# Kernel tuning notes

Hardware: AMD Instinct MI355X
Metric: run time of the kernel (lower is better)

The kernel has to match this reference:

```python
import jax, jax.numpy as jnp
import numpy as np

EMBED_DIM = 1024
NUM_HEADS = 16
HEAD_DIM = EMBED_DIM // NUM_HEADS
FF_DIM = 4096
SPARSITY_FACTOR = 0.1
SPARSITY_THRESHOLD = 0.5
EPS = 1e-5


def layer_norm(x, w, b):
    mu = jnp.mean(x, axis=-1, keepdims=True)
    var = jnp.mean(jnp.square(x - mu), axis=-1, keepdims=True)
    return (x - mu) * jax.lax.rsqrt(var + EPS) * w + b


def setup_inputs() -> dict:
    key = jax.random.key(0)
    ks = jax.random.split(key, 12)
    B, N, C = 8, 1024, EMBED_DIM
    s = 0.02
    return {
        "x": jax.random.normal(ks[0], (B, N, C), jnp.float32),
        "ln1_w": jnp.ones((C,), jnp.float32),
        "ln1_b": jnp.zeros((C,), jnp.float32),
        "qkv_w": jax.random.normal(ks[1], (3 * C, C), jnp.float32) * s,
        "qkv_b": jnp.zeros((3 * C,), jnp.float32),
        "out_w": jax.random.normal(ks[2], (C, C), jnp.float32) * s,
        "out_b": jnp.zeros((C,), jnp.float32),
        "ln2_w": jnp.ones((C,), jnp.float32),
        "ln2_b": jnp.zeros((C,), jnp.float32),
        "w1": jax.random.normal(ks[3], (FF_DIM, C), jnp.float32) * s,
        "b1": jnp.zeros((FF_DIM,), jnp.float32),
        "w2": jax.random.normal(ks[4], (C, FF_DIM), jnp.float32) * s,
        "b2": jnp.zeros((C,), jnp.float32),
        "mask1": jax.random.uniform(ks[5], (B, N, FF_DIM), jnp.float32),
        "mask2": jax.random.uniform(ks[6], (B, N, C), jnp.float32),
        "layer_idx": 0,
    }


def sparse_attention(x, qkv_w, qkv_b, out_w, out_b):
    B, N, C = x.shape
    qkv = (x @ qkv_w.T + qkv_b).reshape(B, N, 3, NUM_HEADS, HEAD_DIM)
    qkv = jnp.transpose(qkv, (2, 0, 3, 1, 4))  # (3,B,H,N,hd)
    q, k, v = qkv[0], qkv[1], qkv[2]
    scale = HEAD_DIM ** (-0.5)
    scores = jnp.einsum("bhnd,bhmd->bhnm", q, k) * scale  # (B,H,N,N)
    k_sparse = int(SPARSITY_FACTOR * N)
    if 0 < k_sparse < N:
        _, idx = jax.lax.top_k(scores, k_sparse)  # (B,H,N,k)
        bi = jnp.arange(B)[:, None, None, None]
        hi = jnp.arange(NUM_HEADS)[None, :, None, None]
        ni = jnp.arange(N)[None, None, :, None]
        mask = jnp.zeros_like(scores).at[bi, hi, ni, idx].set(1.0)
        scores = scores * mask - 1e9 * (1.0 - mask)
    attn = jax.nn.softmax(scores, axis=-1)
    out = jnp.einsum("bhnm,bhmd->bhnd", attn, v)  # (B,H,N,hd)
    out = jnp.transpose(out, (0, 2, 1, 3)).reshape(B, N, C)
    return out @ out_w.T + out_b


def reference(x, ln1_w, ln1_b, qkv_w, qkv_b, out_w, out_b, ln2_w, ln2_b,
              w1, b1, w2, b2, mask1, mask2, layer_idx):
    # Attention block with residual
    x = x + sparse_attention(layer_norm(x, ln1_w, ln1_b), qkv_w, qkv_b, out_w, out_b)
    # Random-masked FFN block with residual
    m1 = (mask1 > SPARSITY_THRESHOLD).astype(x.dtype)
    m2 = (mask2 > SPARSITY_THRESHOLD).astype(x.dtype)
    h = layer_norm(x, ln2_w, ln2_b)
    h = jax.nn.relu((h @ w1.T + b1) * m1)
    h = ((h @ w2.T + b2) * m2)
    x = x + h
    # Symbolic branch: only runs when (layer_idx+1)%4==0 and never modifies x
    # (original ends in `pass`), so it is an identity on the output.
    return x
```

## Files before the change

### kernel.cpp

```cpp
#include <hip/hip_runtime.h>
#include <cstdint>
#include <cstddef>

typedef unsigned short u16;
typedef __bf16 bf16x8 __attribute__((ext_vector_type(8)));
typedef float f32x4 __attribute__((ext_vector_type(4)));

#define GLOBAL_AS __attribute__((address_space(1)))
#define LDS_AS    __attribute__((address_space(3)))

__device__ __forceinline__ float bf2f(u16 v) {
  return __builtin_bit_cast(float, (uint32_t)v << 16);
}
__device__ __forceinline__ u16 f2bf(float f) {
  uint32_t u = __builtin_bit_cast(uint32_t, f);
  u += 0x7FFFu + ((u >> 16) & 1u);
  return (u16)(u >> 16);
}
__device__ __forceinline__ float extload(const void* p, size_t i, int isf) {
  return isf ? ((const float*)p)[i] : bf2f(((const u16*)p)[i]);
}
__device__ __forceinline__ void gl_lds16(const void* g, void* l) {
  __builtin_amdgcn_global_load_lds((const GLOBAL_AS void*)g, (LDS_AS void*)l, 16, 0, 0);
}

__global__ __launch_bounds__(256) void sniff_k(const u16* __restrict__ x, int* __restrict__ flag) {
  const int t = threadIdx.x;
  int cnt = 0;
#pragma unroll
  for (int j = 0; j < 16; ++j) {
    const u16 w = x[t * 16 + j];
    const int e = (w >> 7) & 0xFF;
    cnt += (e >= 0x90) ? 1 : 0;
  }
#pragma unroll
  for (int o = 32; o; o >>= 1) cnt += __shfl_xor(cnt, o);
  __shared__ int red[4];
  if ((t & 63) == 0) red[t >> 6] = cnt;
  __syncthreads();
  if (t == 0) flag[0] = (red[0] + red[1] + red[2] + red[3] > 16) ? 1 : 0;
}

__global__ __launch_bounds__(256) void cvt_k(const void* __restrict__ in, u16* __restrict__ out,
                                             const int* __restrict__ flagp, int n) {
  const int i = (blockIdx.x * 256 + threadIdx.x) * 4;
  if (i >= n) return;
  if (*flagp) {
    const float4 v = *(const float4*)((const float*)in + i);
    out[i] = f2bf(v.x); out[i + 1] = f2bf(v.y); out[i + 2] = f2bf(v.z); out[i + 3] = f2bf(v.w);
  } else {
    *(ushort4*)(out + i) = *(const ushort4*)((const u16*)in + i);
  }
}

template<bool INTF32>
__global__ __launch_bounds__(256) void ln_k(const void* __restrict__ inp,
                                            const void* __restrict__ w,
                                            const void* __restrict__ b,
                                            u16* __restrict__ out,
                                            const int* __restrict__ flagp)
{
  const int isf = *flagp;
  const int row = blockIdx.x;
  const int t = threadIdx.x;
  float x0, x1, x2, x3;
  if (INTF32 || isf) {
    const float4 vv = ((const float4*)((const float*)inp + (size_t)row * 1024))[t];
    x0 = vv.x; x1 = vv.y; x2 = vv.z; x3 = vv.w;
  } else {
    const ushort4 vv = ((const ushort4*)((const u16*)inp + (size_t)row * 1024))[t];
    x0 = bf2f(vv.x); x1 = bf2f(vv.y); x2 = bf2f(vv.z); x3 = bf2f(vv.w);
  }
  float s = x0 + x1 + x2 + x3;
  float sq = x0 * x0 + x1 * x1 + x2 * x2 + x3 * x3;
#pragma unroll
  for (int o = 32; o; o >>= 1) { s += __shfl_xor(s, o); sq += __shfl_xor(sq, o); }
  __shared__ float red[8];
  const int wv = t >> 6;
  if ((t & 63) == 0) { red[wv] = s; red[wv + 4] = sq; }
  __syncthreads();
  s = red[0] + red[1] + red[2] + red[3];
  sq = red[4] + red[5] + red[6] + red[7];
  const float mu = s * (1.0f / 1024.0f);
  const float var = sq * (1.0f / 1024.0f) - mu * mu;
  const float rstd = rsqrtf(var + 1e-5f);
  const int c0 = t * 4;
  u16* o4 = out + (size_t)row * 1024 + c0;
  o4[0] = f2bf((x0 - mu) * rstd * extload(w, c0 + 0, isf) + extload(b, c0 + 0, isf));
  o4[1] = f2bf((x1 - mu) * rstd * extload(w, c0 + 1, isf) + extload(b, c0 + 1, isf));
  o4[2] = f2bf((x2 - mu) * rstd * extload(w, c0 + 2, isf) + extload(b, c0 + 2, isf));
  o4[3] = f2bf((x3 - mu) * rstd * extload(w, c0 + 3, isf) + extload(b, c0 + 3, isf));
}

template<int EPI>
__global__ __launch_bounds__(256, 2) void gemm_bt(
    const u16* __restrict__ A, const u16* __restrict__ B,
    const void* __restrict__ bias, const void* __restrict__ auxb,
    const float* __restrict__ auxf, void* __restrict__ outp,
    int M, int N, int K, const int* __restrict__ flagp)
{
  __shared__ u16 sA[128 * 32];
  __shared__ u16 sB[128 * 32];
  const int t = threadIdx.x;
  const int lane = t & 63;
  const int wv = t >> 6;
  const int wm = (wv >> 1) << 6;
  const int wn = (wv & 1) << 6;
  const int bm = blockIdx.y << 7;
  const int bn = blockIdx.x << 7;

  f32x4 acc[4][4] = {};

  const int ldr = t >> 2;
  const int lseg = t & 3;
  const int fr = lane & 15;
  const int q = lane >> 4;

  for (int kt = 0; kt < K; kt += 32) {
    __syncthreads();
#pragma unroll
    for (int i = 0; i < 2; ++i) {
      const int r = ldr + (i << 6);
      const int sl = lseg ^ ((r >> 1) & 3);
      gl_lds16(A + (size_t)(bm + r) * K + kt + (sl << 3), &sA[(((i << 8) + t) << 3)]);
      gl_lds16(B + (size_t)(bn + r) * K + kt + (sl << 3), &sB[(((i << 8) + t) << 3)]);
    }
    asm volatile("s_waitcnt vmcnt(0)" ::: "memory");
    __syncthreads();

    bf16x8 af[4], bfv[4];
#pragma unroll
    for (int i = 0; i < 4; ++i) {
      const int rr = wm + (i << 4) + fr;
      af[i] = *(const bf16x8*)&sA[(rr << 5) + ((q ^ ((rr >> 1) & 3)) << 3)];
      const int nn = wn + (i << 4) + fr;
      bfv[i] = *(const bf16x8*)&sB[(nn << 5) + ((q ^ ((nn >> 1) & 3)) << 3)];
    }
#pragma unroll
    for (int mi = 0; mi < 4; ++mi)
#pragma unroll
      for (int ni = 0; ni < 4; ++ni)
        acc[mi][ni] = __builtin_amdgcn_mfma_f32_16x16x32_bf16(af[mi], bfv[ni], acc[mi][ni], 0, 0, 0);
  }

  const int isf = *flagp;
#pragma unroll
  for (int mi = 0; mi < 4; ++mi) {
#pragma unroll
    for (int ni = 0; ni < 4; ++ni) {
#pragma unroll
      for (int r = 0; r < 4; ++r) {
        const int gm = bm + wm + (mi << 4) + (q << 2) + r;
        const int gn = bn + wn + (ni << 4) + fr;
        const size_t idx = (size_t)gm * N + gn;
        float v = acc[mi][ni][r] + extload(bias, gn, isf);
        if (EPI == 0) {
          ((u16*)outp)[idx] = f2bf(v);
        } else if (EPI == 1) {
          ((float*)outp)[idx] = v + extload(auxb, idx, isf);
        } else if (EPI == 2) {
          const float keep = extload(auxb, idx, isf) > 0.5f ? 1.0f : 0.0f;
          ((u16*)outp)[idx] = f2bf(fmaxf(v, 0.0f) * keep);
        } else {
          const float keep = extload(auxb, idx, isf) > 0.5f ? 1.0f : 0.0f;
          const float o = auxf[idx] + v * keep;
          if (isf) ((float*)outp)[idx] = o;
          else     ((u16*)outp)[idx] = f2bf(o);
        }
      }
    }
  }
}

__global__ __launch_bounds__(256) void vtrans_k(const u16* __restrict__ qkv,
                                                u16* __restrict__ vt)
{
  __shared__ u16 tile[64][72];
  const int blk = blockIdx.x;
  const int nt = blk & 15, h = (blk >> 4) & 15, b = blk >> 8;
  const int t = threadIdx.x;
#pragma unroll
  for (int it = 0; it < 2; ++it) {
    const int li = it * 256 + t, r = li >> 3, sg = li & 7;
    const uint4 g = *(const uint4*)(qkv + ((size_t)b * 1024 + nt * 64 + r) * 3072 + 2048 + h * 64 + sg * 8);
    *(uint4*)&tile[r][sg * 8] = g;
  }
  __syncthreads();
#pragma unroll
  for (int it = 0; it < 2; ++it) {
    const int li = it * 256 + t, d = li >> 3, sg = li & 7;
    u16 tmp[8];
#pragma unroll
    for (int j = 0; j < 8; ++j) tmp[j] = tile[sg * 8 + j][d];
    *(uint4*)(vt + (((size_t)(b * 16 + h)) * 64 + d) * 1024 + nt * 64 + sg * 8) = *(const uint4*)tmp;
  }
}

__global__ __launch_bounds__(256, 4) void attn_k(const u16* __restrict__ qkv,
                                                 const u16* __restrict__ vt,
                                                 u16* __restrict__ aout)
{
  __shared__ u16 sP[16 * 1032];
  __shared__ float4 red4[4][16];
  __shared__ uint cntb[2][4][16];
  __shared__ uint fcnt[4][16];
  __shared__ float esred[4][16];

  const int t = threadIdx.x;
  const int lane = t & 63;
  const int wv = t >> 6;
  const int bid = blockIdx.x;
  const int sw = ((bid & 7) << 10) | (bid >> 3);
  const int bh = sw >> 6;
  const int rb = sw & 63;
  const int b = bh >> 4, h = bh & 15;
  const size_t row0 = (size_t)b * 1024;
  const int colQ = h * 64;
  const int fr = lane & 15, q = lane >> 4;

  const u16* qrow = qkv + (row0 + rb * 16 + fr) * 3072 + colQ + q * 8;
  const bf16x8 bq0 = *(const bf16x8*)(qrow);
  const bf16x8 bq1 = *(const bf16x8*)(qrow + 32);

  float v2[16][4];
  const u16* kbase = qkv + (row0 + wv * 256 + fr) * 3072 + 1024 + colQ + q * 8;
#pragma unroll
  for (int tt = 0; tt < 16; ++tt) {
    const u16* kp = kbase + (size_t)tt * 16 * 3072;
    const bf16x8 ak0 = *(const bf16x8*)(kp);
    const bf16x8 ak1 = *(const bf16x8*)(kp + 32);
    f32x4 sacc = {};
    sacc = __builtin_amdgcn_mfma_f32_16x16x32_bf16(ak0, bq0, sacc, 0, 0, 0);
    sacc = __builtin_amdgcn_mfma_f32_16x16x32_bf16(ak1, bq1, sacc, 0, 0, 0);
#pragma unroll
    for (int r = 0; r < 4; ++r) v2[tt][r] = sacc[r];
  }

  float mx = v2[0][0], mn = v2[0][0], sm = 0.f, sq = 0.f;
#pragma unroll
  for (int tt = 0; tt < 16; ++tt)
#pragma unroll
    for (int r = 0; r < 4; ++r) {
      const float x = v2[tt][r];
      mx = fmaxf(mx, x); mn = fminf(mn, x); sm += x; sq += x * x;
    }
  mx = fmaxf(mx, __shfl_xor(mx, 16)); mx = fmaxf(mx, __shfl_xor(mx, 32));
  mn = fminf(mn, __shfl_xor(mn, 16)); mn = fminf(mn, __shfl_xor(mn, 32));
  sm += __shfl_xor(sm, 16); sm += __shfl_xor(sm, 32);
  sq += __shfl_xor(sq, 16); sq += __shfl_xor(sq, 32);
  if (lane < 16) red4[wv][fr] = make_float4(mx, mn, sm, sq);
  __syncthreads();
  {
    const float4 a0 = red4[0][fr], a1 = red4[1][fr], a2 = red4[2][fr], a3 = red4[3][fr];
    mx = fmaxf(fmaxf(a0.x, a1.x), fmaxf(a2.x, a3.x));
    mn = fminf(fminf(a0.y, a1.y), fminf(a2.y, a3.y));
    sm = a0.z + a1.z + a2.z + a3.z;
    sq = a0.w + a1.w + a2.w + a3.w;
  }

  float lo, hi, tcur, texact = 0.f;
  int nlo = 1024, nhi = 0;
  bool done = false;
  {
    const float mu = sm * (1.0f / 1024.0f);
    const float var = fmaxf(sq * (1.0f / 1024.0f) - mu * mu, 0.0f);
    const float sd = sqrtf(var + 1e-20f);
    lo = mn - fabsf(mn) * 1e-6f - 1e-12f;
    hi = mx + fabsf(mx) * 1e-6f + 1e-12f;
    const float t0 = mu + 1.2816f * sd;
    const float wdt = hi - lo;
    tcur = fminf(fmaxf(t0, lo + 0.02f * wdt), hi - 0.02f * wdt);
  }

  for (int it = 0; it < 10; ++it) {
    if (__ballot(!done) == 0ull) break;
    int c_ = 0;
#pragma unroll
    for (int tt = 0; tt < 16; ++tt)
#pragma unroll
      for (int r = 0; r < 4; ++r) c_ += (v2[tt][r] >= tcur) ? 1 : 0;
    c_ += __shfl_xor(c_, 16); c_ += __shfl_xor(c_, 32);
    if (lane < 16) cntb[it & 1][wv][fr] = (uint)c_;
    __syncthreads();
    const int cc = (int)(cntb[it & 1][0][fr] + cntb[it & 1][1][fr] +
                         cntb[it & 1][2][fr] + cntb[it & 1][3][fr]);
    if (!done) {
      if (cc == 102) { done = true; texact = tcur; }
      else if (cc > 102) { lo = tcur; nlo = cc; }
      else { hi = tcur; nhi = cc; }
      float tn;
      if (it & 1) tn = 0.5f * (lo + hi);
      else {
        const float den = (float)(nlo - nhi);
        tn = lo + (hi - lo) * ((float)(nlo - 102) / den);
      }
      const float wdt = hi - lo;
      tcur = fminf(fmaxf(tn, lo + 0.02f * wdt), hi - 0.02f * wdt);
    }
  }

  uint64_t kmask = 0ull;
  const uint64_t anymask = __ballot(!done);
  if (anymask == 0ull) {
#pragma unroll
    for (int tt = 0; tt < 16; ++tt)
#pragma unroll
      for (int r = 0; r < 4; ++r)
        if (v2[tt][r] >= texact) kmask |= 1ull << (tt * 4 + r);
  } else {
    const float thr = done ? texact : hi;
    int bc = 0;
#pragma unroll
    for (int tt = 0; tt < 16; ++tt)
#pragma unroll
      for (int r = 0; r < 4; ++r) {
        const float x = v2[tt][r];
        if (x >= thr) kmask |= 1ull << (tt * 4 + r);
        bc += (!done && x >= lo && x < hi) ? 1 : 0;
      }
    int bw = bc + __shfl_xor(bc, 16);
    bw += __shfl_xor(bw, 32);
    if (lane < 16) fcnt[wv][fr] = (uint)bw;
    __syncthreads();
    if (!done) {
      int pre = 0;
#pragma unroll
      for (int w = 0; w < 4; ++w) if (w < wv) pre += (int)fcnt[w][fr];
#pragma unroll
      for (int qq = 0; qq < 3; ++qq) {
        const int ov = __shfl(bc, fr + 16 * qq);
        if (qq < q) pre += ov;
      }
      const int need = 102 - nhi;
#pragma unroll
      for (int tt = 0; tt < 16; ++tt)
#pragma unroll
        for (int r = 0; r < 4; ++r) {
          const float x = v2[tt][r];
          if (x >= lo && x < hi) {
            if (pre < need) kmask |= 1ull << (tt * 4 + r);
            ++pre;
          }
        }
    }
  }

  const float CEXP = 0.125f * 1.44269504f;
  float es = 0.f;
#pragma unroll
  for (int tt = 0; tt < 16; ++tt)
#pragma unroll
    for (int r = 0; r < 4; ++r) {
      const float e = ((kmask >> (tt * 4 + r)) & 1ull) ? exp2f((v2[tt][r] - mx) * CEXP) : 0.0f;
      v2[tt][r] = e;
      es += e;
    }
  es += __shfl_xor(es, 16); es += __shfl_xor(es, 32);
  if (lane < 16) esred[wv][fr] = es;
  __syncthreads();
  const float inv = 1.0f / (esred[0][fr] + esred[1][fr] + esred[2][fr] + esred[3][fr]);

  u16* prow = sP + (size_t)fr * 1032 + wv * 256;
#pragma unroll
  for (int tt = 0; tt < 16; ++tt) {
#pragma unroll
    for (int rp = 0; rp < 2; ++rp) {
      const u16 p0 = f2bf(v2[tt][2 * rp] * inv);
      const u16 p1 = f2bf(v2[tt][2 * rp + 1] * inv);
      *(uint*)(prow + tt * 16 + q * 4 + 2 * rp) = (uint)p0 | ((uint)p1 << 16);
    }
  }
  __syncthreads();

  const u16* vtb = vt + (((size_t)(b * 16 + h)) * 64 + wv * 16 + fr) * 1024 + q * 8;
  const u16* pbase = sP + fr * 1032 + q * 8;
  f32x4 oacc = {};
#pragma unroll
  for (int c = 0; c < 16; ++c) {
    const bf16x8 ap0 = *(const bf16x8*)(pbase + c * 64);
    const bf16x8 ap1 = *(const bf16x8*)(pbase + c * 64 + 32);
    const bf16x8 bv0 = *(const bf16x8*)(vtb + c * 64);
    const bf16x8 bv1 = *(const bf16x8*)(vtb + c * 64 + 32);
    oacc = __builtin_amdgcn_mfma_f32_16x16x32_bf16(ap0, bv0, oacc, 0, 0, 0);
    oacc = __builtin_amdgcn_mfma_f32_16x16x32_bf16(ap1, bv1, oacc, 0, 0, 0);
  }
#pragma unroll
  for (int r = 0; r < 4; ++r)
    aout[(row0 + rb * 16 + q * 4 + r) * 1024 + colQ + wv * 16 + fr] = f2bf(oacc[r]);
}

extern "C" void kernel_launch(void* const* d_in, const int* in_sizes, int n_in,
                              void* d_out, int out_size, void* d_ws, size_t ws_size,
                              hipStream_t stream)
{
  (void)in_sizes; (void)n_in; (void)out_size; (void)ws_size;
  const void* x     = d_in[0];
  const void* ln1w  = d_in[1];
  const void* ln1b  = d_in[2];
  const void* qkvw  = d_in[3];
  const void* qkvb  = d_in[4];
  const void* outw  = d_in[5];
  const void* outb  = d_in[6];
  const void* ln2w  = d_in[7];
  const void* ln2b  = d_in[8];
  const void* w1    = d_in[9];
  const void* b1    = d_in[10];
  const void* w2    = d_in[11];
  const void* b2    = d_in[12];
  const void* mask1 = d_in[13];
  const void* mask2 = d_in[14];

  char* ws = (char*)d_ws;
  const size_t MB = 1ull << 20;
  u16*   xn1    = (u16*)(ws);
  u16*   qkv    = (u16*)(ws + 16 * MB);
  u16*   xn2    = qkv;
  u16*   w1c    = (u16*)(ws + 32 * MB);
  u16*   w2c    = (u16*)(ws + 40 * MB);
  float* x2     = (float*)(ws + 64 * MB);
  u16*   h1     = (u16*)(ws + 96 * MB);
  u16*   wq     = (u16*)(ws + 96 * MB);
  u16*   wo     = (u16*)(ws + 102 * MB);
  u16*   vt     = (u16*)(ws + 104 * MB);
  int*   flagp  = (int*)(ws + 160 * MB);
  u16*   attn_o = xn1;

  sniff_k<<<1, 256, 0, stream>>>((const u16*)x, flagp);
  cvt_k<<<3072, 256, 0, stream>>>(qkvw, wq, flagp, 3072 * 1024);
  cvt_k<<<1024, 256, 0, stream>>>(outw, wo, flagp, 1024 * 1024);

  ln_k<false><<<8192, 256, 0, stream>>>(x, ln1w, ln1b, xn1, flagp);
  gemm_bt<0><<<dim3(24, 64), 256, 0, stream>>>(xn1, wq, qkvb, nullptr, nullptr, qkv, 8192, 3072, 1024, flagp);
  vtrans_k<<<2048, 256, 0, stream>>>(qkv, vt);
  attn_k<<<8192, 256, 0, stream>>>(qkv, vt, attn_o);
  gemm_bt<1><<<dim3(8, 64), 256, 0, stream>>>(attn_o, wo, outb, x, nullptr, x2, 8192, 1024, 1024, flagp);

  cvt_k<<<4096, 256, 0, stream>>>(w1, w1c, flagp, 4096 * 1024);
  cvt_k<<<4096, 256, 0, stream>>>(w2, w2c, flagp, 4096 * 1024);

  ln_k<true><<<8192, 256, 0, stream>>>(x2, ln2w, ln2b, xn2, flagp);
  gemm_bt<2><<<dim3(32, 64), 256, 0, stream>>>(xn2, w1c, b1, mask1, nullptr, h1, 8192, 4096, 1024, flagp);
  gemm_bt<3><<<dim3(8, 64), 256, 0, stream>>>(h1, w2c, b2, mask2, x2, d_out, 8192, 1024, 4096, flagp);
}
```

Before: 1.030 ms.

## Use two-threshold top-k search, drop max/min reduction, defer softmax normalization

The attention kernel's top-k threshold search now tests two candidate thresholds per pass (a secant and a bisection point) and packs both counts into one 32-bit word, cutting the maximum number of passes and block barriers. The per-row max/min reduction is gone: the search bounds and the softmax shift come from mean ± 6 sigma instead. Softmax normalization moves to after the PV MFMA, which removes one barrier, and the first V tiles are prefetched before the barrier. The risk is exp overflow or a wrong bracket if a score lies beyond 6 sigma, and bf16 rounding of unnormalized probabilities may change accuracy slightly.

New measurement: 1.032 ms. No clear change (+0.2%).

```diff
diff --git a/kernel.cpp b/kernel.cpp
--- a/kernel.cpp
+++ b/kernel.cpp
@@ -201,7 +201,7 @@
                                                  u16* __restrict__ aout)
 {
   __shared__ u16 sP[16 * 1032];
-  __shared__ float4 red4[4][16];
+  __shared__ float2 red2[4][16];
   __shared__ uint cntb[2][4][16];
   __shared__ uint fcnt[4][16];
   __shared__ float esred[4][16];
@@ -236,157 +236,173 @@
     for (int r = 0; r < 4; ++r) v2[tt][r] = sacc[r];
   }
 
-  float mx = v2[0][0], mn = v2[0][0], sm = 0.f, sq = 0.f;
+  float sm = 0.f, sq = 0.f;
 #pragma unroll
   for (int tt = 0; tt < 16; ++tt)
 #pragma unroll
     for (int r = 0; r < 4; ++r) {
       const float x = v2[tt][r];
-      mx = fmaxf(mx, x); mn = fminf(mn, x); sm += x; sq += x * x;
-    }
-  mx = fmaxf(mx, __shfl_xor(mx, 16)); mx = fmaxf(mx, __shfl_xor(mx, 32));
-  mn = fminf(mn, __shfl_xor(mn, 16)); mn = fminf(mn, __shfl_xor(mn, 32));
+      sm += x; sq += x * x;
+    }
   sm += __shfl_xor(sm, 16); sm += __shfl_xor(sm, 32);
   sq += __shfl_xor(sq, 16); sq += __shfl_xor(sq, 32);
-  if (lane < 16) red4[wv][fr] = make_float4(mx, mn, sm, sq);
+  if (lane < 16) red2[wv][fr] = make_float2(sm, sq);
   __syncthreads();
   {
-    const float4 a0 = red4[0][fr], a1 = red4[1][fr], a2 = red4[2][fr], a3 = red4[3][fr];
-    mx = fmaxf(fmaxf(a0.x, a1.x), fmaxf(a2.x, a3.x));
-    mn = fminf(fminf(a0.y, a1.y), fminf(a2.y, a3.y));
-    sm = a0.z + a1.z + a2.z + a3.z;
-    sq = a0.w + a1.w + a2.w + a3.w;
-  }
-
-  float lo, hi, tcur, texact = 0.f;
+    const float2 a0 = red2[0][fr], a1 = red2[1][fr], a2 = red2[2][fr], a3 = red2[3][fr];
+    sm = a0.x + a1.x + a2.x + a3.x;
+    sq = a0.y + a1.y + a2.y + a3.y;
+  }
+
+  const float mu = sm * (1.0f / 1024.0f);
+  const float var = fmaxf(sq * (1.0f / 1024.0f) - mu * mu, 0.0f);
+  const float sd = sqrtf(var + 1e-20f);
+  float lo = mu - 6.0f * sd;
+  float hi = mu + 6.0f * sd;
+  const float M = hi;
   int nlo = 1024, nhi = 0;
   bool done = false;
-  {
-    const float mu = sm * (1.0f / 1024.0f);
-    const float var = fmaxf(sq * (1.0f / 1024.0f) - mu * mu, 0.0f);
-    const float sd = sqrtf(var + 1e-20f);
-    lo = mn - fabsf(mn) * 1e-6f - 1e-12f;
-    hi = mx + fabsf(mx) * 1e-6f + 1e-12f;
-    const float t0 = mu + 1.2816f * sd;
-    const float wdt = hi - lo;
-    tcur = fminf(fmaxf(t0, lo + 0.02f * wdt), hi - 0.02f * wdt);
-  }
-
-  for (int it = 0; it < 10; ++it) {
+  float texact = 0.f;
+  float t1 = mu + 1.10f * sd;
+  float t2 = mu + 1.50f * sd;
+
+  for (int it = 0; it < 6; ++it) {
     if (__ballot(!done) == 0ull) break;
-    int c_ = 0;
-#pragma unroll
-    for (int tt = 0; tt < 16; ++tt)
-#pragma unroll
-      for (int r = 0; r < 4; ++r) c_ += (v2[tt][r] >= tcur) ? 1 : 0;
-    c_ += __shfl_xor(c_, 16); c_ += __shfl_xor(c_, 32);
-    if (lane < 16) cntb[it & 1][wv][fr] = (uint)c_;
-    __syncthreads();
-    const int cc = (int)(cntb[it & 1][0][fr] + cntb[it & 1][1][fr] +
-                         cntb[it & 1][2][fr] + cntb[it & 1][3][fr]);
-    if (!done) {
-      if (cc == 102) { done = true; texact = tcur; }
-      else if (cc > 102) { lo = tcur; nlo = cc; }
-      else { hi = tcur; nhi = cc; }
-      float tn;
-      if (it & 1) tn = 0.5f * (lo + hi);
-      else {
-        const float den = (float)(nlo - nhi);
-        tn = lo + (hi - lo) * ((float)(nlo - 102) / den);
-      }
-      const float wdt = hi - lo;
-      tcur = fminf(fmaxf(tn, lo + 0.02f * wdt), hi - 0.02f * wdt);
-    }
-  }
-
-  uint64_t kmask = 0ull;
-  const uint64_t anymask = __ballot(!done);
-  if (anymask == 0ull) {
-#pragma unroll
-    for (int tt = 0; tt < 16; ++tt)
-#pragma unroll
-      for (int r = 0; r < 4; ++r)
-        if (v2[tt][r] >= texact) kmask |= 1ull << (tt * 4 + r);
-  } else {
-    const float thr = done ? texact : hi;
-    int bc = 0;
+    int c1 = 0, c2 = 0;
 #pragma unroll
     for (int tt = 0; tt < 16; ++tt)
 #pragma unroll
       for (int r = 0; r < 4; ++r) {
         const float x = v2[tt][r];
-        if (x >= thr) kmask |= 1ull << (tt * 4 + r);
-        bc += (!done && x >= lo && x < hi) ? 1 : 0;
-      }
-    int bw = bc + __shfl_xor(bc, 16);
-    bw += __shfl_xor(bw, 32);
-    if (lane < 16) fcnt[wv][fr] = (uint)bw;
+        c1 += (x >= t1) ? 1 : 0;
+        c2 += (x >= t2) ? 1 : 0;
+      }
+    uint pk = ((uint)c1 << 16) | (uint)c2;
+    pk += (uint)__shfl_xor((int)pk, 16); pk += (uint)__shfl_xor((int)pk, 32);
+    if (lane < 16) cntb[it & 1][wv][fr] = pk;
+    __syncthreads();
+    const uint cc = cntb[it & 1][0][fr] + cntb[it & 1][1][fr] +
+                    cntb[it & 1][2][fr] + cntb[it & 1][3][fr];
+    const int cc1 = (int)(cc >> 16), cc2 = (int)(cc & 0xFFFFu);
+    if (!done) {
+      if (cc1 == 102) { done = true; texact = t1; }
+      else if (cc2 == 102) { done = true; texact = t2; }
+      else if (cc2 > 102) { lo = t2; nlo = cc2; }
+      else if (cc1 < 102) { hi = t1; nhi = cc1; }
+      else { lo = t1; nlo = cc1; hi = t2; nhi = cc2; }
+      const float wdt = hi - lo;
+      const float ts = lo + wdt * ((float)(nlo - 102) / (float)(nlo - nhi));
+      const float tm = lo + 0.5f * wdt;
+      t1 = fminf(ts, tm); t2 = fmaxf(ts, tm);
+      t1 = fminf(fmaxf(t1, lo + 0.02f * wdt), hi - 0.02f * wdt);
+      t2 = fminf(fmaxf(t2, lo + 0.02f * wdt), hi - 0.02f * wdt);
+    }
+  }
+
+  const float CEXP = 0.125f * 1.44269504f;
+  const uint64_t anymask = __ballot(!done);
+  float es = 0.f;
+  if (anymask == 0ull) {
+#pragma unroll
+    for (int tt = 0; tt < 16; ++tt)
+#pragma unroll
+      for (int r = 0; r < 4; ++r) {
+        const float x = v2[tt][r];
+        const float e = (x >= texact) ? exp2f((x - M) * CEXP) : 0.0f;
+        v2[tt][r] = e; es += e;
+      }
+  } else {
+    uint64_t kmask = 0ull;
+    const float thr = done ? texact : hi;
+    int bc = 0, tc = 0;
+#pragma unroll
+    for (int tt = 0; tt < 16; ++tt)
+#pragma unroll
+      for (int r = 0; r < 4; ++r) {
+        const float x = v2[tt][r];
+        if (x >= thr) { kmask |= 1ull << (tt * 4 + r); ++tc; }
+        bc += (!done && x >= lo && x < thr) ? 1 : 0;
+      }
+    uint pk2 = ((uint)tc << 16) | (uint)bc;
+    pk2 += (uint)__shfl_xor((int)pk2, 16); pk2 += (uint)__shfl_xor((int)pk2, 32);
+    if (lane < 16) fcnt[wv][fr] = pk2;
     __syncthreads();
     if (!done) {
+      const uint ft = fcnt[0][fr] + fcnt[1][fr] + fcnt[2][fr] + fcnt[3][fr];
+      const int tct = (int)(ft >> 16);
       int pre = 0;
 #pragma unroll
-      for (int w = 0; w < 4; ++w) if (w < wv) pre += (int)fcnt[w][fr];
+      for (int w = 0; w < 4; ++w) if (w < wv) pre += (int)(fcnt[w][fr] & 0xFFFFu);
 #pragma unroll
       for (int qq = 0; qq < 3; ++qq) {
         const int ov = __shfl(bc, fr + 16 * qq);
         if (qq < q) pre += ov;
       }
-      const int need = 102 - nhi;
+      const int need = 102 - tct;
 #pragma unroll
       for (int tt = 0; tt < 16; ++tt)
 #pragma unroll
         for (int r = 0; r < 4; ++r) {
           const float x = v2[tt][r];
-          if (x >= lo && x < hi) {
+          if (x >= lo && x < thr) {
             if (pre < need) kmask |= 1ull << (tt * 4 + r);
             ++pre;
           }
         }
     }
-  }
-
-  const float CEXP = 0.125f * 1.44269504f;
-  float es = 0.f;
-#pragma unroll
-  for (int tt = 0; tt < 16; ++tt)
-#pragma unroll
-    for (int r = 0; r < 4; ++r) {
-      const float e = ((kmask >> (tt * 4 + r)) & 1ull) ? exp2f((v2[tt][r] - mx) * CEXP) : 0.0f;
-      v2[tt][r] = e;
-      es += e;
-    }
+#pragma unroll
+    for (int tt = 0; tt < 16; ++tt)
+#pragma unroll
+      for (int r = 0; r < 4; ++r) {
+        const float e = ((kmask >> (tt * 4 + r)) & 1ull)
+                        ? exp2f((v2[tt][r] - M) * CEXP) : 0.0f;
+        v2[tt][r] = e; es += e;
+      }
+  }
+
   es += __shfl_xor(es, 16); es += __shfl_xor(es, 32);
   if (lane < 16) esred[wv][fr] = es;
+
+  u16* prow = sP + (size_t)fr * 1032 + wv * 256;
+#pragma unroll
+  for (int tt = 0; tt < 16; ++tt) {
+    uint2 pw;
+    pw.x = (uint)f2bf(v2[tt][0]) | ((uint)f2bf(v2[tt][1]) << 16);
+    pw.y = (uint)f2bf(v2[tt][2]) | ((uint)f2bf(v2[tt][3]) << 16);
+    *(uint2*)(prow + tt * 16 + q * 4) = pw;
+  }
+
+  const u16* vtb = vt + (((size_t)(b * 16 + h)) * 64 + wv * 16 + fr) * 1024 + q * 8;
+  bf16x8 pv[8];
+#pragma unroll
+  for (int c = 0; c < 4; ++c) {
+    pv[2 * c]     = *(const bf16x8*)(vtb + c * 64);
+    pv[2 * c + 1] = *(const bf16x8*)(vtb + c * 64 + 32);
+  }
   __syncthreads();
-  const float inv = 1.0f / (esred[0][fr] + esred[1][fr] + esred[2][fr] + esred[3][fr]);
-
-  u16* prow = sP + (size_t)fr * 1032 + wv * 256;
-#pragma unroll
-  for (int tt = 0; tt < 16; ++tt) {
-#pragma unroll
-    for (int rp = 0; rp < 2; ++rp) {
-      const u16 p0 = f2bf(v2[tt][2 * rp] * inv);
-      const u16 p1 = f2bf(v2[tt][2 * rp + 1] * inv);
-      *(uint*)(prow + tt * 16 + q * 4 + 2 * rp) = (uint)p0 | ((uint)p1 << 16);
-    }
-  }
-  __syncthreads();
-
-  const u16* vtb = vt + (((size_t)(b * 16 + h)) * 64 + wv * 16 + fr) * 1024 + q * 8;
+
   const u16* pbase = sP + fr * 1032 + q * 8;
   f32x4 oacc = {};
 #pragma unroll
   for (int c = 0; c < 16; ++c) {
     const bf16x8 ap0 = *(const bf16x8*)(pbase + c * 64);
     const bf16x8 ap1 = *(const bf16x8*)(pbase + c * 64 + 32);
-    const bf16x8 bv0 = *(const bf16x8*)(vtb + c * 64);
-    const bf16x8 bv1 = *(const bf16x8*)(vtb + c * 64 + 32);
+    bf16x8 bv0, bv1;
+    if (c < 4) { bv0 = pv[2 * c]; bv1 = pv[2 * c + 1]; }
+    else {
+      bv0 = *(const bf16x8*)(vtb + c * 64);
+      bv1 = *(const bf16x8*)(vtb + c * 64 + 32);
+    }
     oacc = __builtin_amdgcn_mfma_f32_16x16x32_bf16(ap0, bv0, oacc, 0, 0, 0);
     oacc = __builtin_amdgcn_mfma_f32_16x16x32_bf16(ap1, bv1, oacc, 0, 0, 0);
   }
-#pragma unroll
-  for (int r = 0; r < 4; ++r)
-    aout[(row0 + rb * 16 + q * 4 + r) * 1024 + colQ + wv * 16 + fr] = f2bf(oacc[r]);
+
+#pragma unroll
+  for (int r = 0; r < 4; ++r) {
+    const int qq = q * 4 + r;
+    const float est = esred[0][qq] + esred[1][qq] + esred[2][qq] + esred[3][qq];
+    aout[(row0 + rb * 16 + qq) * 1024 + colQ + wv * 16 + fr] = f2bf(oacc[r] / est);
+  }
 }
 
 extern "C" void kernel_launch(void* const* d_in, const int* in_sizes, int n_in,
```

## Double-buffer LDS tiles in bf16 GEMM to overlap global loads with MFMA

Applied to the files above, without the earlier changes.

The GEMM now keeps two LDS buffers for the A and B tiles. It issues the global-to-LDS loads for the next K tile before running MFMAs on the current one, then waits and syncs once per iteration. This is meant to hide global memory latency behind matrix math and remove one of the two barriers per K step. In exchange LDS use doubles to 32 KB per block, which may limit occupancy, and there is a possible hazard if the LDS reads are not finished before the buffer is overwritten two iterations later.

After: 1.026 ms. About the same (-0.4%).

```diff
diff --git a/kernel.cpp b/kernel.cpp
--- a/kernel.cpp
+++ b/kernel.cpp
@@ -99,8 +99,8 @@
     const float* __restrict__ auxf, void* __restrict__ outp,
     int M, int N, int K, const int* __restrict__ flagp)
 {
-  __shared__ u16 sA[128 * 32];
-  __shared__ u16 sB[128 * 32];
+  __shared__ u16 sA[2][128 * 32];
+  __shared__ u16 sB[2][128 * 32];
   const int t = threadIdx.x;
   const int lane = t & 63;
   const int wv = t >> 6;
@@ -116,32 +116,51 @@
   const int fr = lane & 15;
   const int q = lane >> 4;
 
-  for (int kt = 0; kt < K; kt += 32) {
-    __syncthreads();
-#pragma unroll
-    for (int i = 0; i < 2; ++i) {
-      const int r = ldr + (i << 6);
-      const int sl = lseg ^ ((r >> 1) & 3);
-      gl_lds16(A + (size_t)(bm + r) * K + kt + (sl << 3), &sA[(((i << 8) + t) << 3)]);
-      gl_lds16(B + (size_t)(bn + r) * K + kt + (sl << 3), &sB[(((i << 8) + t) << 3)]);
-    }
-    asm volatile("s_waitcnt vmcnt(0)" ::: "memory");
-    __syncthreads();
+  const int nt = K >> 5;
+
+#define STAGE(buf, kt)                                                          \
+  {                                                                             \
+    _Pragma("unroll")                                                           \
+    for (int i = 0; i < 2; ++i) {                                               \
+      const int r = ldr + (i << 6);                                             \
+      const int sl = lseg ^ ((r >> 1) & 3);                \
+      gl_lds16(A + (size_t)(bm + r) * K + (kt) + (sl << 3),                     \
+               &sA[buf][(((i << 8) + t) << 3)]);                                \
+      gl_lds16(B + (size_t)(bn + r) * K + (kt) + (sl << 3),                     \
+               &sB[buf][(((i << 8) + t) << 3)]);                                \
+    }                                                                           \
+  }
+
+  STAGE(0, 0);
+  asm volatile("s_waitcnt vmcnt(0)" ::: "memory");
+  __syncthreads();
+
+  int cur = 0;
+  for (int kt_i = 0; kt_i < nt; ++kt_i) {
+    const bool more = (kt_i + 1 < nt);
+    if (more) STAGE(cur ^ 1, (kt_i + 1) << 5);
 
     bf16x8 af[4], bfv[4];
 #pragma unroll
     for (int i = 0; i < 4; ++i) {
       const int rr = wm + (i << 4) + fr;
-      af[i] = *(const bf16x8*)&sA[(rr << 5) + ((q ^ ((rr >> 1) & 3)) << 3)];
+      af[i] = *(const bf16x8*)&sA[cur][(rr << 5) + ((q ^ ((rr >> 1) & 3)) << 3)];
       const int nn = wn + (i << 4) + fr;
-      bfv[i] = *(const bf16x8*)&sB[(nn << 5) + ((q ^ ((nn >> 1) & 3)) << 3)];
+      bfv[i] = *(const bf16x8*)&sB[cur][(nn << 5) + ((q ^ ((nn >> 1) & 3)) << 3)];
     }
 #pragma unroll
     for (int mi = 0; mi < 4; ++mi)
 #pragma unroll
       for (int ni = 0; ni < 4; ++ni)
         acc[mi][ni] = __builtin_amdgcn_mfma_f32_16x16x32_bf16(af[mi], bfv[ni], acc[mi][ni], 0, 0, 0);
-  }
+
+    if (more) {
+      asm volatile("s_waitcnt vmcnt(0)" ::: "memory");
+      __syncthreads();
+      cur ^= 1;
+    }
+  }
+#undef STAGE
 
   const int isf = *flagp;
 #pragma unroll
```
